# Kernel optimization log

Measured on AMD Instinct MI355X. Metric: run time of the kernel, lower is better.

Reference implementation:

```python
import jax, jax.numpy as jnp
import numpy as np

B, T, C, H, L, V = 2, 1024, 768, 12, 6, 32000
HS = C // H  # head size 64
EPS = 1e-5


def _ln(x, g, b):
    m = jnp.mean(x, axis=-1, keepdims=True)
    v = jnp.var(x, axis=-1, keepdims=True)
    return (x - m) * jax.lax.rsqrt(v + EPS) * g + b


def setup_inputs() -> dict:
    key = jax.random.key(0)
    ks = iter(jax.random.split(key, 32))
    s = lambda *sh: jax.random.normal(next(ks), sh, jnp.float32) * 0.02
    return {
        "idx": jax.random.randint(next(ks), (B, T), 0, V),
        "tok_emb": s(V, C),
        "pos_emb": s(T, C),
        "Wq": s(L, H, C, HS), "Wk": s(L, H, C, HS), "Wv": s(L, H, C, HS),
        "Wp": s(L, C, C), "bp": jnp.zeros((L, C), jnp.float32),
        "ln1g": jnp.ones((L, C), jnp.float32), "ln1b": jnp.zeros((L, C), jnp.float32),
        "ln2g": jnp.ones((L, C), jnp.float32), "ln2b": jnp.zeros((L, C), jnp.float32),
        "W1": s(L, C, 4 * C), "b1": jnp.zeros((L, 4 * C), jnp.float32),
        "W2": s(L, 4 * C, C), "b2": jnp.zeros((L, C), jnp.float32),
        "lnfg": jnp.ones((C,), jnp.float32), "lnfb": jnp.zeros((C,), jnp.float32),
        "Wh": s(C, V), "bh": jnp.zeros((V,), jnp.float32),
    }


def reference(idx, tok_emb, pos_emb, Wq, Wk, Wv, Wp, bp, ln1g, ln1b, ln2g, ln2b,
              W1, b1, W2, b2, lnfg, lnfb, Wh, bh):
    x = tok_emb[idx] + pos_emb[None, :, :]  # [B,T,C]
    # NOTE: original scales by full embed dim C ** -0.5 (not head_size)
    scale = C ** (-0.5)
    causal = jnp.tril(jnp.ones((T, T), bool))

    def block(x, p):
        wq, wk, wv, wp, bpj, g1, be1, g2, be2, w1, bb1, w2, bb2 = p
        h = _ln(x, g1, be1)
        q = jnp.einsum('btc,hcs->bhts', h, wq)
        k = jnp.einsum('btc,hcs->bhts', h, wk)
        v = jnp.einsum('btc,hcs->bhts', h, wv)
        wei = jnp.einsum('bhts,bhus->bhtu', q, k) * scale
        wei = jnp.where(causal, wei, -jnp.inf)
        wei = jax.nn.softmax(wei, axis=-1)
        o = jnp.einsum('bhtu,bhus->bhts', wei, v)
        o = o.transpose(0, 2, 1, 3).reshape(x.shape[0], T, C)  # concat heads
        x = x + o @ wp + bpj
        h2 = _ln(x, g2, be2)
        x = x + jax.nn.relu(h2 @ w1 + bb1) @ w2 + bb2
        return x, None

    x, _ = jax.lax.scan(block, x, (Wq, Wk, Wv, Wp, bp, ln1g, ln1b, ln2g, ln2b, W1, b1, W2, b2))
    logits = _ln(x, lnfg, lnfb) @ Wh + bh  # [B,T,V]
    return logits
```

## Files before the change

### kernel.cpp

```cpp
#include <hip/hip_runtime.h>

#define B_ 2
#define T_ 1024
#define C_ 768
#define H_ 12
#define L_ 6
#define V_ 32000
#define HS_ 64
#define M_ (B_*T_)
#define C4_ (4*C_)
#define NVC_ 6400

typedef __attribute__((ext_vector_type(8))) short short8;
typedef __attribute__((ext_vector_type(4))) float f32x4;

__device__ __forceinline__ float b2f(unsigned short u) {
  union { unsigned int i; float f; } x; x.i = ((unsigned int)u) << 16; return x.f;
}
__device__ __forceinline__ unsigned short f2b(float f) {
  unsigned int u = __builtin_bit_cast(unsigned int, f);
  u += 0x7fffu + ((u >> 16) & 1u);
  return (unsigned short)(u >> 16);
}

__device__ __forceinline__ void gload16(const unsigned short* g, unsigned short* l) {
  __builtin_amdgcn_global_load_lds(
      (const __attribute__((address_space(1))) unsigned int*)g,
      (__attribute__((address_space(3))) unsigned int*)l, 16, 0, 0);
}

__global__ __launch_bounds__(256) void transpose_f2b(const float* __restrict__ in,
                                                     unsigned short* __restrict__ out,
                                                     int ldi, int ldo, size_t zi, size_t zo) {
  __shared__ unsigned short tile[32][33];
  in  += zi * blockIdx.z;
  out += zo * blockIdx.z;
  int c0 = blockIdx.x * 32, r0 = blockIdx.y * 32;
  int tx = threadIdx.x & 31, ty = threadIdx.x >> 5;
  #pragma unroll
  for (int j = 0; j < 32; j += 8)
    tile[ty + j][tx] = f2b(in[(size_t)(r0 + ty + j) * ldi + c0 + tx]);
  __syncthreads();
  #pragma unroll
  for (int j = 0; j < 32; j += 8)
    out[(size_t)(c0 + ty + j) * ldo + r0 + tx] = tile[tx][ty + j];
}

__global__ __launch_bounds__(256) void transpose_qkvp(const float* __restrict__ Wq,
                                                      const float* __restrict__ Wk,
                                                      const float* __restrict__ Wv,
                                                      const float* __restrict__ Wp,
                                                      unsigned short* __restrict__ out) {
  __shared__ unsigned short tile[32][33];
  int z = blockIdx.z;
  const float* in; unsigned short* o; int ldi; int cbase;
  if (z < 36) {
    int which = z / H_, hh = z % H_;
    in = (which == 0 ? Wq : which == 1 ? Wk : Wv) + (size_t)hh * C_ * HS_;
    o = out + (size_t)which * C_ * C_ + (size_t)hh * HS_ * C_;
    ldi = HS_; cbase = 0;
  } else {
    int ch = z - 36;
    in = Wp; ldi = C_; cbase = ch * 64;
    o = out + (size_t)3 * C_ * C_ + (size_t)ch * 64 * C_;
  }
  int c0 = blockIdx.x * 32, r0 = blockIdx.y * 32;
  int tx = threadIdx.x & 31, ty = threadIdx.x >> 5;
  #pragma unroll
  for (int j = 0; j < 32; j += 8)
    tile[ty + j][tx] = f2b(in[(size_t)(r0 + ty + j) * ldi + cbase + c0 + tx]);
  __syncthreads();
  #pragma unroll
  for (int j = 0; j < 32; j += 8)
    o[(size_t)(c0 + ty + j) * C_ + r0 + tx] = tile[tx][ty + j];
}

__global__ __launch_bounds__(256) void embed_kernel(const int* __restrict__ idx,
                                                    const float* __restrict__ tok,
                                                    const float* __restrict__ pos,
                                                    float* __restrict__ x) {
  int m = blockIdx.x;
  int t = m & (T_ - 1);
  int tk = idx[m];
  #pragma unroll
  for (int i = 0; i < 3; ++i) {
    int c = threadIdx.x + i * 256;
    x[(size_t)m * C_ + c] = tok[(size_t)tk * C_ + c] + pos[(size_t)t * C_ + c];
  }
}

__global__ __launch_bounds__(256) void ln_kernel(const float* __restrict__ x,
                                                 const float* __restrict__ g,
                                                 const float* __restrict__ bta,
                                                 unsigned short* __restrict__ h) {
  int m = blockIdx.x;
  const float* xr = x + (size_t)m * C_;
  float v[3], s = 0.f, ss = 0.f;
  #pragma unroll
  for (int i = 0; i < 3; ++i) {
    v[i] = xr[threadIdx.x + i * 256];
    s += v[i]; ss += v[i] * v[i];
  }
  #pragma unroll
  for (int off = 32; off; off >>= 1) { s += __shfl_xor(s, off); ss += __shfl_xor(ss, off); }
  __shared__ float red[8];
  int wave = threadIdx.x >> 6, lane = threadIdx.x & 63;
  if (lane == 0) { red[wave] = s; red[4 + wave] = ss; }
  __syncthreads();
  s  = red[0] + red[1] + red[2] + red[3];
  ss = red[4] + red[5] + red[6] + red[7];
  float mean = s * (1.f / C_);
  float var  = fmaxf(ss * (1.f / C_) - mean * mean, 0.f);
  float rstd = rsqrtf(var + 1e-5f);
  #pragma unroll
  for (int i = 0; i < 3; ++i) {
    int c = threadIdx.x + i * 256;
    h[(size_t)m * C_ + c] = f2b((v[i] - mean) * rstd * g[c] + bta[c]);
  }
}

__global__ __launch_bounds__(256) void attn_mfma(const unsigned short* __restrict__ q,
                                                 const unsigned short* __restrict__ k,
                                                 const unsigned short* __restrict__ v,
                                                 unsigned short* __restrict__ o) {
  const float scale = 0.03608439182435161f;
  __shared__ __align__(16) unsigned short Ks[64 * 72];
  __shared__ __align__(16) unsigned short Vt[64 * 72];
  __shared__ __align__(16) unsigned short Ps[4][16 * 72];

  int tid = threadIdx.x;
  int lane = tid & 63, wave = tid >> 6;
  int rl = lane & 15, kgrp = lane >> 4, koff = kgrp * 8;
  int bh = blockIdx.y;
  int hh = bh % H_, bb = bh / H_;
  size_t base = (size_t)bb * T_ * C_ + (size_t)hh * HS_;

  for (int pass = 0; pass < 2; ++pass) {
    int qt = pass ? (15 - (int)blockIdx.x) : (int)blockIdx.x;

    short8 qf0 = *(const short8*)&q[base + (size_t)(qt * 64 + wave * 16 + rl) * C_ + koff];
    short8 qf1 = *(const short8*)&q[base + (size_t)(qt * 64 + wave * 16 + rl) * C_ + 32 + koff];

    float m_[4], l_[4];
    f32x4 oacc[4];
    #pragma unroll
    for (int r = 0; r < 4; ++r) { m_[r] = -INFINITY; l_[r] = 0.f; }
    #pragma unroll
    for (int j = 0; j < 4; ++j) oacc[j] = (f32x4){0.f, 0.f, 0.f, 0.f};

    short8 kreg[2], vreg[2];
    #pragma unroll
    for (int i = 0; i < 2; ++i) {
      int e = tid + i * 256;
      kreg[i] = *(const short8*)&k[base + (size_t)(e >> 3) * C_ + (e & 7) * 8];
      vreg[i] = *(const short8*)&v[base + (size_t)(e >> 3) * C_ + (e & 7) * 8];
    }

    for (int kt = 0; kt <= qt; ++kt) {
      #pragma unroll
      for (int i = 0; i < 2; ++i) {
        int e = tid + i * 256, row = e >> 3, c8 = e & 7;
        *(short8*)&Ks[row * 72 + c8 * 8] = kreg[i];
      }
      #pragma unroll
      for (int i = 0; i < 2; ++i) {
        int e = tid + i * 256, kk = e >> 3, d8 = (e & 7) * 8;
        short8 vv = vreg[i];
        #pragma unroll
        for (int t2 = 0; t2 < 8; ++t2) {
          int ii = (t2 + tid) & 7;
          Vt[(d8 + ii) * 72 + kk] = vv[ii];
        }
      }
      __syncthreads();

      if (kt < qt) {
        #pragma unroll
        for (int i = 0; i < 2; ++i) {
          int e = tid + i * 256;
          kreg[i] = *(const short8*)&k[base + (size_t)((kt + 1) * 64 + (e >> 3)) * C_ + (e & 7) * 8];
          vreg[i] = *(const short8*)&v[base + (size_t)((kt + 1) * 64 + (e >> 3)) * C_ + (e & 7) * 8];
        }
      }

      f32x4 s[4];
      #pragma unroll
      for (int j = 0; j < 4; ++j) s[j] = (f32x4){0.f, 0.f, 0.f, 0.f};
      __builtin_amdgcn_s_setprio(1);
      #pragma unroll
      for (int j = 0; j < 4; ++j) {
        short8 b0 = *(const short8*)&Ks[(j * 16 + rl) * 72 + koff];
        short8 b1 = *(const short8*)&Ks[(j * 16 + rl) * 72 + 32 + koff];
        s[j] = __builtin_amdgcn_mfma_f32_16x16x32_bf16(qf0, b0, s[j], 0, 0, 0);
        s[j] = __builtin_amdgcn_mfma_f32_16x16x32_bf16(qf1, b1, s[j], 0, 0, 0);
      }
      __builtin_amdgcn_s_setprio(0);

      bool diag = (kt == qt);
      #pragma unroll
      for (int j = 0; j < 4; ++j)
        #pragma unroll
        for (int r = 0; r < 4; ++r) {
          float sv = s[j][r] * scale;
          if (diag) {
            int urow = j * 16 + rl, qrow = wave * 16 + kgrp * 4 + r;
            if (urow > qrow) sv = -INFINITY;
          }
          s[j][r] = sv;
        }

      float corr[4], rs[4];
      #pragma unroll
      for (int r = 0; r < 4; ++r) {
        float mrow = fmaxf(fmaxf(s[0][r], s[1][r]), fmaxf(s[2][r], s[3][r]));
        #pragma unroll
        for (int off = 8; off; off >>= 1) mrow = fmaxf(mrow, __shfl_xor(mrow, off));
        float mnew = fmaxf(m_[r], mrow);
        corr[r] = __expf(m_[r] - mnew);
        m_[r] = mnew;
      }
      #pragma unroll
      for (int r = 0; r < 4; ++r) rs[r] = 0.f;
      #pragma unroll
      for (int j = 0; j < 4; ++j)
        #pragma unroll
        for (int r = 0; r < 4; ++r) {
          float p = (s[j][r] == -INFINITY) ? 0.f : __expf(s[j][r] - m_[r]);
          s[j][r] = p;
          rs[r] += p;
        }
      #pragma unroll
      for (int r = 0; r < 4; ++r) {
        #pragma unroll
        for (int off = 8; off; off >>= 1) rs[r] += __shfl_xor(rs[r], off);
        l_[r] = l_[r] * corr[r] + rs[r];
      }
      #pragma unroll
      for (int j = 0; j < 4; ++j)
        #pragma unroll
        for (int r = 0; r < 4; ++r) oacc[j][r] *= corr[r];

      #pragma unroll
      for (int j = 0; j < 4; ++j)
        #pragma unroll
        for (int r = 0; r < 4; ++r)
          Ps[wave][(kgrp * 4 + r) * 72 + j * 16 + rl] = f2b(s[j][r]);

      short8 pa0 = *(const short8*)&Ps[wave][rl * 72 + koff];
      short8 pa1 = *(const short8*)&Ps[wave][rl * 72 + 32 + koff];
      __builtin_amdgcn_s_setprio(1);
      #pragma unroll
      for (int j = 0; j < 4; ++j) {
        short8 b0 = *(const short8*)&Vt[(j * 16 + rl) * 72 + koff];
        short8 b1 = *(const short8*)&Vt[(j * 16 + rl) * 72 + 32 + koff];
        oacc[j] = __builtin_amdgcn_mfma_f32_16x16x32_bf16(pa0, b0, oacc[j], 0, 0, 0);
        oacc[j] = __builtin_amdgcn_mfma_f32_16x16x32_bf16(pa1, b1, oacc[j], 0, 0, 0);
      }
      __builtin_amdgcn_s_setprio(0);
      __syncthreads();
    }

    #pragma unroll
    for (int j = 0; j < 4; ++j)
      #pragma unroll
      for (int r = 0; r < 4; ++r) {
        int qrow = wave * 16 + kgrp * 4 + r;
        o[base + (size_t)(qt * 64 + qrow) * C_ + j * 16 + rl] = f2b(oacc[j][r] / l_[r]);
      }
  }
}

template<int BM, int BN, int EPI, bool MFAST, bool SWZ>
__global__ __launch_bounds__(256) void gemm_bt(const unsigned short* __restrict__ A,
                                               const unsigned short* __restrict__ Bt,
                                               const float* __restrict__ bias,
                                               unsigned short* __restrict__ outb,
                                               float* __restrict__ outf,
                                               int M, int N, int K, int ldO,
                                               size_t zBt, size_t zOut, int nMt) {
  constexpr int BK = 32;
  __shared__ __align__(16) unsigned short As[BM * BK];
  __shared__ __align__(16) unsigned short Bs[BN * BK];
  constexpr int FM = BM / 32, FN = BN / 32;

  int tid = threadIdx.x;
  int lane = tid & 63, wave = tid >> 6;
  int wr = wave >> 1, wc = wave & 1;
  int m0, n0;
  if (SWZ) {
    int nwg = gridDim.x, wg = blockIdx.x;
    int qq = nwg >> 3, rr = nwg & 7;
    int xcd = wg & 7, off = wg >> 3;
    int wgid = (xcd < rr ? xcd * (qq + 1) : rr * (qq + 1) + (xcd - rr) * qq) + off;
    m0 = (wgid % nMt) * BM;
    n0 = (wgid / nMt) * BN;
  } else {
    m0 = (MFAST ? blockIdx.x : blockIdx.y) * BM;
    n0 = (MFAST ? blockIdx.y : blockIdx.x) * BN;
  }
  int rl = lane & 15, koff = (lane >> 4) * 8;
  Bt += zBt * blockIdx.z;

  int srow = lane >> 2, sseg = (lane & 3) * 8;

  f32x4 acc[FM][FN] = {};

  for (int k0 = 0; k0 < K; k0 += BK) {
    #pragma unroll
    for (int i = 0; i < BM / 64; ++i) {
      int r = i * 64 + wave * 16;
      gload16(&A[(size_t)(m0 + r + srow) * K + k0 + sseg], &As[r * BK]);
    }
    #pragma unroll
    for (int i = 0; i < BN / 64; ++i) {
      int r = i * 64 + wave * 16;
      gload16(&Bt[(size_t)(n0 + r + srow) * K + k0 + sseg], &Bs[r * BK]);
    }
    __syncthreads();

    short8 af[FM], bfr[FN];
    #pragma unroll
    for (int i = 0; i < FM; ++i)
      af[i] = *(const short8*)&As[(wr * (BM / 2) + i * 16 + rl) * BK + koff];
    #pragma unroll
    for (int j = 0; j < FN; ++j)
      bfr[j] = *(const short8*)&Bs[(wc * (BN / 2) + j * 16 + rl) * BK + koff];
    #pragma unroll
    for (int i = 0; i < FM; ++i)
      #pragma unroll
      for (int j = 0; j < FN; ++j)
        acc[i][j] = __builtin_amdgcn_mfma_f32_16x16x32_bf16(af[i], bfr[j], acc[i][j], 0, 0, 0);
    __syncthreads();
  }

  int rbase = (lane >> 4) * 4;
  #pragma unroll
  for (int i = 0; i < FM; ++i) {
    #pragma unroll
    for (int j = 0; j < FN; ++j) {
      #pragma unroll
      for (int r = 0; r < 4; ++r) {
        int m = m0 + wr * (BM / 2) + i * 16 + rbase + r;
        int n = n0 + wc * (BN / 2) + j * 16 + (lane & 15);
        float val = acc[i][j][r];
        if (bias) val += bias[n];
        if (EPI == 0)      (outb + zOut * blockIdx.z)[(size_t)m * ldO + n] = f2b(val);
        else if (EPI == 1) (outb + zOut * blockIdx.z)[(size_t)m * ldO + n] = f2b(fmaxf(val, 0.f));
        else if (EPI == 2) (outf + zOut * blockIdx.z)[(size_t)m * ldO + n] += val;
        else               (outf + zOut * blockIdx.z)[(size_t)m * ldO + n] = val;
      }
    }
  }
}

extern "C" void kernel_launch(void* const* d_in, const int* in_sizes, int n_in,
                              void* d_out, int out_size, void* d_ws, size_t ws_size,
                              hipStream_t stream) {
  const int*   idx  = (const int*)d_in[0];
  const float* tok  = (const float*)d_in[1];
  const float* pos  = (const float*)d_in[2];
  const float* Wq   = (const float*)d_in[3];
  const float* Wk   = (const float*)d_in[4];
  const float* Wv   = (const float*)d_in[5];
  const float* Wp   = (const float*)d_in[6];
  const float* bp   = (const float*)d_in[7];
  const float* ln1g = (const float*)d_in[8];
  const float* ln1b = (const float*)d_in[9];
  const float* ln2g = (const float*)d_in[10];
  const float* ln2b = (const float*)d_in[11];
  const float* W1   = (const float*)d_in[12];
  const float* b1   = (const float*)d_in[13];
  const float* W2   = (const float*)d_in[14];
  const float* b2   = (const float*)d_in[15];
  const float* lnfg = (const float*)d_in[16];
  const float* lnfb = (const float*)d_in[17];
  const float* Wh   = (const float*)d_in[18];
  const float* bh   = (const float*)d_in[19];

  float* out = (float*)d_out;

  const size_t MC = (size_t)M_ * C_;
  const size_t fixed = MC*4 + MC*2 + MC*2*4;
  const size_t need_chunk = fixed + (size_t)NVC_*C_*2;
  const size_t need_full  = fixed + (size_t)V_*C_*2;
  if (ws_size < need_chunk) return;
  const bool full_head = (ws_size >= need_full);

  char* p = (char*)d_ws;
  float*          x   = (float*)p;            p += MC*4;
  unsigned short* h   = (unsigned short*)p;   p += MC*2;
  unsigned short* qb  = (unsigned short*)p;   p += MC*2;
  unsigned short* kb  = (unsigned short*)p;   p += MC*2;
  unsigned short* vb  = (unsigned short*)p;   p += MC*2;
  unsigned short* ob  = (unsigned short*)p;   p += MC*2;
  unsigned short* WT  = (unsigned short*)p;
  unsigned short* mid = qb;

  unsigned short* WqT = WT;
  unsigned short* WpT = WT + (size_t)3*C_*C_;
  unsigned short* W12T = WT;

  embed_kernel<<<M_, 256, 0, stream>>>(idx, tok, pos, x);

  for (int l = 0; l < L_; ++l) {
    size_t wo  = (size_t)l * C_ * C_;
    size_t wo4 = (size_t)l * C_ * C4_;
    size_t woq = (size_t)l * H_ * C_ * HS_;

    transpose_qkvp<<<dim3(HS_/32, C_/32, 48), 256, 0, stream>>>(Wq + woq, Wk + woq, Wv + woq, Wp + wo, WqT);

    ln_kernel<<<M_, 256, 0, stream>>>(x, ln1g + (size_t)l*C_, ln1b + (size_t)l*C_, h);
    gemm_bt<64,64,0,false,false><<<dim3(C_/64, M_/64, 3), 256, 0, stream>>>(h, WqT, nullptr, qb, nullptr,
                                                                            M_, C_, C_, C_, (size_t)C_*C_, MC, 0);
    attn_mfma<<<dim3(8, B_*H_), 256, 0, stream>>>(qb, kb, vb, ob);
    gemm_bt<64,64,2,false,false><<<dim3(C_/64, M_/64), 256, 0, stream>>>(ob, WpT, bp + (size_t)l*C_, nullptr, x,
                                                                         M_, C_, C_, C_, 0, 0, 0);

    ln_kernel<<<M_, 256, 0, stream>>>(x, ln2g + (size_t)l*C_, ln2b + (size_t)l*C_, h);
    transpose_f2b<<<dim3(C4_/32, C_/32, 1), 256, 0, stream>>>(W1 + wo4, W12T, C4_, C_, 0, 0);
    gemm_bt<128,128,1,true,true><<<dim3((M_/128)*(C4_/128)), 256, 0, stream>>>(h, W12T, b1 + (size_t)l*C4_, mid, nullptr,
                                                                               M_, C4_, C_, C4_, 0, 0, M_/128);
    transpose_f2b<<<dim3(C_/32, C4_/32, 1), 256, 0, stream>>>(W2 + wo4, W12T, C_, C4_, 0, 0);
    gemm_bt<64,64,2,true,true><<<dim3((M_/64)*(C_/64)), 256, 0, stream>>>(mid, W12T, b2 + (size_t)l*C_, nullptr, x,
                                                                          M_, C_, C4_, C_, 0, 0, M_/64);
  }

  ln_kernel<<<M_, 256, 0, stream>>>(x, lnfg, lnfb, h);
  if (full_head) {
    transpose_f2b<<<dim3(V_/32, C_/32, 1), 256, 0, stream>>>(Wh, WT, V_, C_, 0, 0);
    gemm_bt<128,128,3,true,true><<<dim3((M_/128)*(V_/128)), 256, 0, stream>>>(
        h, WT, bh, nullptr, out, M_, V_, C_, V_, 0, 0, M_/128);
  } else {
    for (int ci = 0; ci < V_/NVC_; ++ci) {
      transpose_f2b<<<dim3(NVC_/32, C_/32, 1), 256, 0, stream>>>(Wh + (size_t)ci*NVC_, WT, V_, C_, 0, 0);
      gemm_bt<128,128,3,true,true><<<dim3((M_/128)*(NVC_/128)), 256, 0, stream>>>(
          h, WT, bh + (size_t)ci*NVC_, nullptr, out + (size_t)ci*NVC_, M_, NVC_, C_, V_, 0, 0, M_/128);
    }
  }
}
```

Before: 1.310 ms.

## Double GEMM K-tile with XOR-swizzled LDS and use one wave per LayerNorm row

The GEMM K step grows from 32 to 64 and LDS tiles use an XOR swizzle on 16-byte segments to avoid bank conflicts. Each iteration now issues two MFMAs per fragment pair, which halves the barriers and loop overhead. LayerNorm now gives each row to one wavefront and handles four rows per block, removing the shared-memory reduction and the __syncthreads. The costs are double the LDS per block (which may cut occupancy) and extra registers for the fragments.

New measurement: 1.212 ms. 7.5% less time.

```diff
diff --git a/kernel.cpp b/kernel.cpp
--- a/kernel.cpp
+++ b/kernel.cpp
@@ -93,28 +93,23 @@
                                                  const float* __restrict__ g,
                                                  const float* __restrict__ bta,
                                                  unsigned short* __restrict__ h) {
-  int m = blockIdx.x;
+  int wave = threadIdx.x >> 6, lane = threadIdx.x & 63;
+  int m = blockIdx.x * 4 + wave;
   const float* xr = x + (size_t)m * C_;
-  float v[3], s = 0.f, ss = 0.f;
-  #pragma unroll
-  for (int i = 0; i < 3; ++i) {
-    v[i] = xr[threadIdx.x + i * 256];
+  float v[12], s = 0.f, ss = 0.f;
+  #pragma unroll
+  for (int i = 0; i < 12; ++i) {
+    v[i] = xr[lane + i * 64];
     s += v[i]; ss += v[i] * v[i];
   }
   #pragma unroll
   for (int off = 32; off; off >>= 1) { s += __shfl_xor(s, off); ss += __shfl_xor(ss, off); }
-  __shared__ float red[8];
-  int wave = threadIdx.x >> 6, lane = threadIdx.x & 63;
-  if (lane == 0) { red[wave] = s; red[4 + wave] = ss; }
-  __syncthreads();
-  s  = red[0] + red[1] + red[2] + red[3];
-  ss = red[4] + red[5] + red[6] + red[7];
   float mean = s * (1.f / C_);
   float var  = fmaxf(ss * (1.f / C_) - mean * mean, 0.f);
   float rstd = rsqrtf(var + 1e-5f);
   #pragma unroll
-  for (int i = 0; i < 3; ++i) {
-    int c = threadIdx.x + i * 256;
+  for (int i = 0; i < 12; ++i) {
+    int c = lane + i * 64;
     h[(size_t)m * C_ + c] = f2b((v[i] - mean) * rstd * g[c] + bta[c]);
   }
 }
@@ -278,7 +273,7 @@
                                                float* __restrict__ outf,
                                                int M, int N, int K, int ldO,
                                                size_t zBt, size_t zOut, int nMt) {
-  constexpr int BK = 32;
+  constexpr int BK = 64;
   __shared__ __align__(16) unsigned short As[BM * BK];
   __shared__ __align__(16) unsigned short Bs[BN * BK];
   constexpr int FM = BM / 32, FN = BN / 32;
@@ -298,42 +293,54 @@
     m0 = (MFAST ? blockIdx.x : blockIdx.y) * BM;
     n0 = (MFAST ? blockIdx.y : blockIdx.x) * BN;
   }
-  int rl = lane & 15, koff = (lane >> 4) * 8;
+  int rl = lane & 15, kgrp = lane >> 4;
   Bt += zBt * blockIdx.z;
 
-  int srow = lane >> 2, sseg = (lane & 3) * 8;
+  int srow = lane >> 3;
+  int scol = ((lane & 7) ^ srow) * 8;
+
+  int pc0 = ((kgrp)     ^ (rl & 7)) * 8;
+  int pc1 = ((4 + kgrp) ^ (rl & 7)) * 8;
 
   f32x4 acc[FM][FN] = {};
 
   for (int k0 = 0; k0 < K; k0 += BK) {
     #pragma unroll
-    for (int i = 0; i < BM / 64; ++i) {
-      int r = i * 64 + wave * 16;
-      gload16(&A[(size_t)(m0 + r + srow) * K + k0 + sseg], &As[r * BK]);
-    }
-    #pragma unroll
-    for (int i = 0; i < BN / 64; ++i) {
-      int r = i * 64 + wave * 16;
-      gload16(&Bt[(size_t)(n0 + r + srow) * K + k0 + sseg], &Bs[r * BK]);
+    for (int i = 0; i < BM / 32; ++i) {
+      int r = i * 32 + wave * 8;
+      gload16(&A[(size_t)(m0 + r + srow) * K + k0 + scol], &As[r * BK]);
+    }
+    #pragma unroll
+    for (int i = 0; i < BN / 32; ++i) {
+      int r = i * 32 + wave * 8;
+      gload16(&Bt[(size_t)(n0 + r + srow) * K + k0 + scol], &Bs[r * BK]);
     }
     __syncthreads();
 
-    short8 af[FM], bfr[FN];
+    short8 af0[FM], af1[FM], bf0[FN], bf1[FN];
+    #pragma unroll
+    for (int i = 0; i < FM; ++i) {
+      int row = wr * (BM / 2) + i * 16 + rl;
+      af0[i] = *(const short8*)&As[row * BK + pc0];
+      af1[i] = *(const short8*)&As[row * BK + pc1];
+    }
+    #pragma unroll
+    for (int j = 0; j < FN; ++j) {
+      int row = wc * (BN / 2) + j * 16 + rl;
+      bf0[j] = *(const short8*)&Bs[row * BK + pc0];
+      bf1[j] = *(const short8*)&Bs[row * BK + pc1];
+    }
     #pragma unroll
     for (int i = 0; i < FM; ++i)
-      af[i] = *(const short8*)&As[(wr * (BM / 2) + i * 16 + rl) * BK + koff];
-    #pragma unroll
-    for (int j = 0; j < FN; ++j)
-      bfr[j] = *(const short8*)&Bs[(wc * (BN / 2) + j * 16 + rl) * BK + koff];
-    #pragma unroll
-    for (int i = 0; i < FM; ++i)
-      #pragma unroll
-      for (int j = 0; j < FN; ++j)
-        acc[i][j] = __builtin_amdgcn_mfma_f32_16x16x32_bf16(af[i], bfr[j], acc[i][j], 0, 0, 0);
+      #pragma unroll
+      for (int j = 0; j < FN; ++j) {
+        acc[i][j] = __builtin_amdgcn_mfma_f32_16x16x32_bf16(af0[i], bf0[j], acc[i][j], 0, 0, 0);
+        acc[i][j] = __builtin_amdgcn_mfma_f32_16x16x32_bf16(af1[i], bf1[j], acc[i][j], 0, 0, 0);
+      }
     __syncthreads();
   }
 
-  int rbase = (lane >> 4) * 4;
+  int rbase = kgrp * 4;
   #pragma unroll
   for (int i = 0; i < FM; ++i) {
     #pragma unroll
@@ -341,7 +348,7 @@
       #pragma unroll
       for (int r = 0; r < 4; ++r) {
         int m = m0 + wr * (BM / 2) + i * 16 + rbase + r;
-        int n = n0 + wc * (BN / 2) + j * 16 + (lane & 15);
+        int n = n0 + wc * (BN / 2) + j * 16 + rl;
         float val = acc[i][j][r];
         if (bias) val += bias[n];
         if (EPI == 0)      (outb + zOut * blockIdx.z)[(size_t)m * ldO + n] = f2b(val);
@@ -409,14 +416,14 @@
 
     transpose_qkvp<<<dim3(HS_/32, C_/32, 48), 256, 0, stream>>>(Wq + woq, Wk + woq, Wv + woq, Wp + wo, WqT);
 
-    ln_kernel<<<M_, 256, 0, stream>>>(x, ln1g + (size_t)l*C_, ln1b + (size_t)l*C_, h);
+    ln_kernel<<<M_/4, 256, 0, stream>>>(x, ln1g + (size_t)l*C_, ln1b + (size_t)l*C_, h);
     gemm_bt<64,64,0,false,false><<<dim3(C_/64, M_/64, 3), 256, 0, stream>>>(h, WqT, nullptr, qb, nullptr,
                                                                             M_, C_, C_, C_, (size_t)C_*C_, MC, 0);
     attn_mfma<<<dim3(8, B_*H_), 256, 0, stream>>>(qb, kb, vb, ob);
     gemm_bt<64,64,2,false,false><<<dim3(C_/64, M_/64), 256, 0, stream>>>(ob, WpT, bp + (size_t)l*C_, nullptr, x,
                                                                          M_, C_, C_, C_, 0, 0, 0);
 
-    ln_kernel<<<M_, 256, 0, stream>>>(x, ln2g + (size_t)l*C_, ln2b + (size_t)l*C_, h);
+    ln_kernel<<<M_/4, 256, 0, stream>>>(x, ln2g + (size_t)l*C_, ln2b + (size_t)l*C_, h);
     transpose_f2b<<<dim3(C4_/32, C_/32, 1), 256, 0, stream>>>(W1 + wo4, W12T, C4_, C_, 0, 0);
     gemm_bt<128,128,1,true,true><<<dim3((M_/128)*(C4_/128)), 256, 0, stream>>>(h, W12T, b1 + (size_t)l*C4_, mid, nullptr,
                                                                                M_, C4_, C_, C4_, 0, 0, M_/128);
@@ -425,7 +432,7 @@
                                                                           M_, C_, C4_, C_, 0, 0, M_/64);
   }
 
-  ln_kernel<<<M_, 256, 0, stream>>>(x, lnfg, lnfb, h);
+  ln_kernel<<<M_/4, 256, 0, stream>>>(x, lnfg, lnfb, h);
   if (full_head) {
     transpose_f2b<<<dim3(V_/32, C_/32, 1), 256, 0, stream>>>(Wh, WT, V_, C_, 0, 0);
     gemm_bt<128,128,3,true,true><<<dim3((M_/128)*(V_/128)), 256, 0, stream>>>(
```
